# Kernel tuning notes

Measured on AMD Instinct MI355X. Metric: run time of the kernel, lower is better.

## Reference

```python
import jax, jax.numpy as jnp
import numpy as np

B, L, D, K, O, DM = 32, 512, 32, 6, 192, 512
Q = 0.75
EPS = 1e-6
BN_EPS = 1e-5


def _torch_median(a, axis):
    # torch.median returns the LOWER of the two middle values for even n
    n = a.shape[axis]
    s = jnp.sort(a, axis=axis)
    return jnp.take(s, jnp.array([(n - 1) // 2]), axis=axis)


def setup_inputs() -> dict:
    key = jax.random.key(0)
    ks = jax.random.split(key, 5)
    return {
        "x": jax.random.normal(ks[0], (B, L, D), jnp.float32),
        "x_date": jax.random.normal(ks[1], (B, L, D, K), jnp.float32),
        "y_date": jax.random.normal(ks[2], (B, O, D, K), jnp.float32),
        "mlp_w1": jax.random.normal(ks[3], (L, DM), jnp.float32) * 0.02,
        "mlp_b1": jnp.zeros((DM,), jnp.float32),
        "mlp_w2": jax.random.normal(ks[4], (DM, 2), jnp.float32) * 0.02,
        "mlp_b2": jnp.zeros((2,), jnp.float32),
        "bn_gamma": jnp.ones((D,), jnp.float32),
        "bn_beta": jnp.zeros((D,), jnp.float32),
    }


def reference(x, x_date, y_date, mlp_w1, mlp_b1, mlp_w2, mlp_b2, bn_gamma, bn_beta):
    k = x_date.shape[-1]
    # robust location/scale (median + interquantile range), reduced over time dim 1
    med_true = _torch_median(x, 1)                 # (B,1,D)
    med_map = _torch_median(x_date, 1)             # (B,1,D,K)
    std_true = (jnp.quantile(x, Q, axis=1, keepdims=True)
                - jnp.quantile(x, 1.0 - Q, axis=1, keepdims=True) + EPS)   # (B,1,D)
    std_map = (jnp.quantile(x_date, Q, axis=1, keepdims=True)
               - jnp.quantile(x_date, 1.0 - Q, axis=1, keepdims=True) + EPS)  # (B,1,D,K)
    x_date_map = (x_date - med_map) / std_map * std_true[..., None] + med_true[..., None]
    y_date_map = (y_date - med_map) / std_map * std_true[..., None] + med_true[..., None]

    # cross-attention over time with tiny contraction dim k
    scores = jnp.einsum('bldk,bodk->bdlo', x_date_map, y_date_map)  # (B,D,L,O)
    A = jax.nn.softmax(scores / jnp.sqrt(jnp.float32(k)), axis=-2)  # softmax over L
    V = jnp.einsum('bld,bdlo->bdo', x, A)                           # (B,D,O)

    # BatchNorm1d(d_feature) in training mode: batch stats over (B, O); dropout = identity (eval)
    mu = jnp.mean(V, axis=(0, 2), keepdims=True)
    var = jnp.var(V, axis=(0, 2), keepdims=True)
    y = (V - mu) * jax.lax.rsqrt(var + BN_EPS) * bn_gamma[None, :, None] + bn_beta[None, :, None]
    y = jnp.transpose(y, (0, 2, 1))                                 # (B,O,D)

    # softmax-gated fusion MLP over the time axis
    error = x - x_date_map.mean(-1)                                 # (B,L,D)
    h = jax.nn.gelu(jnp.einsum('bld,lm->bdm', error, mlp_w1) + mlp_b1, approximate=False)
    w = jax.nn.softmax(h @ mlp_w2 + mlp_b2, axis=-1)                # (B,D,2)

    y_map = jnp.stack([y_date_map.mean(-1), y], axis=-1)            # (B,O,D,2)
    pred = jnp.sum(y_map * w[:, None], axis=-1)                     # (B,O,D)
    return pred
```

## Files before the change

### kernel.cpp

```cpp
#include <hip/hip_runtime.h>
#include <math.h>

#define BB 32
#define LL 512
#define DD 32
#define KK 6
#define OO 192
#define DM 512

typedef __fp16 h2 __attribute__((ext_vector_type(2)));
union F2H { float f; h2 h; };
__device__ __forceinline__ float asF(h2 h) { F2H u; u.h = h; return u.f; }
__device__ __forceinline__ h2 asH(float f) { F2H u; u.f = f; return u.h; }

typedef short bf16x8 __attribute__((ext_vector_type(8)));
typedef float f4 __attribute__((ext_vector_type(4)));
union U16x8 { uint4 u; bf16x8 h; };

__device__ __forceinline__ unsigned short f2bf(float x) {
  unsigned int u = __float_as_uint(x);
  u = (u + 0x7FFF + ((u >> 16) & 1)) >> 16;
  return (unsigned short)u;
}

#define MOVDPP(x, ctrl) \
  __int_as_float(__builtin_amdgcn_mov_dpp(__float_as_int(x), ctrl, 0xf, 0xf, true))

#define CSTR2 524
#define XD0   0
#define XV0   6288
#define MEDO  7336
#define STDO  7350
#define SAO   7364
#define SCO   7376
#define BNR   7388
#define PK    0
#define DENB  4200
#define NUMB  4968
#define LDSF  7404

__device__ __forceinline__ void sort512(float v[8], int lane) {
  #pragma unroll
  for (int k = 2; k <= 512; k <<= 1) {
    #pragma unroll
    for (int j = k >> 1; j > 0; j >>= 1) {
      if (j >= 8) {
        int jj = j >> 3;
        bool lower = (lane & jj) == 0;
        bool asc = ((lane << 3) & k) == 0;
        bool keepmin = (asc == lower);
        #pragma unroll
        for (int r = 0; r < 8; ++r) {
          float o;
          if (jj == 1)      o = MOVDPP(v[r], 0xB1);
          else if (jj == 2) o = MOVDPP(v[r], 0x4E);
          else if (jj == 8) o = MOVDPP(v[r], 0x128);
          else              o = __shfl_xor(v[r], jj);
          v[r] = keepmin ? fminf(v[r], o) : fmaxf(v[r], o);
        }
      } else {
        #pragma unroll
        for (int r = 0; r < 8; ++r) {
          if ((r & j) == 0) {
            int r2 = r | j;
            bool asc = (((lane << 3) | r) & k) == 0;
            float a = v[r], b = v[r2];
            float lo = fminf(a, b), hi = fmaxf(a, b);
            v[r]  = asc ? lo : hi;
            v[r2] = asc ? hi : lo;
          }
        }
      }
    }
  }
}

__global__ __launch_bounds__(256) void fused_kernel(
    const float* __restrict__ x, const float* __restrict__ x_date,
    const float* __restrict__ y_date, const float* __restrict__ w1,
    float* __restrict__ V, float* __restrict__ ymean,
    float* __restrict__ bnp, unsigned short* __restrict__ errb,
    unsigned short* __restrict__ w1t) {
  __shared__ float lds[LDSF];
  int orig = blockIdx.x;
  int tid = threadIdx.x, lane = tid & 63, wv = tid >> 6;

  if (orig >= 512) {
    float* tw = lds;
    int id = orig - 512;
    int l0 = (id & 7) * 64, m0 = (id >> 3) * 64;
    #pragma unroll
    for (int it = 0; it < 4; ++it) {
      int f = tid + it * 256;
      int row = f >> 4, c4 = f & 15;
      float4 v = ((const float4*)(w1 + (size_t)(l0 + row) * DM + m0))[c4];
      float* p = &tw[row * 68 + c4 * 4];
      p[0] = v.x; p[1] = v.y; p[2] = v.z; p[3] = v.w;
    }
    __syncthreads();
    unsigned int* w1t32 = (unsigned int*)w1t;
    #pragma unroll
    for (int it = 0; it < 8; ++it) {
      int f = tid + it * 256;
      int mr = f >> 5, c = f & 31;
      float a = tw[(c * 2 + 0) * 68 + mr];
      float b = tw[(c * 2 + 1) * 68 + mr];
      unsigned int u = (unsigned int)f2bf(a) | ((unsigned int)f2bf(b) << 16);
      w1t32[(size_t)(m0 + mr) * (DM / 2) + (l0 >> 1) + c] = u;
    }
    return;
  }

  int xcd = orig & 7, idx = orig >> 3;
  int b = (xcd << 2) | (idx >> 4);
  int d0 = (idx & 15) << 1;

  const float* xs = x_date + (size_t)b * LL * 192 + d0 * 6;
  #pragma unroll
  for (int it = 0; it < 6; ++it) {
    int f = tid + it * 256;
    int row = f / 3, c4 = f % 3;
    float4 v = ((const float4*)(xs + (size_t)row * 192))[c4];
    int col = c4 * 4;
    lds[XD0 + (col + 0) * CSTR2 + row] = v.x;
    lds[XD0 + (col + 1) * CSTR2 + row] = v.y;
    lds[XD0 + (col + 2) * CSTR2 + row] = v.z;
    lds[XD0 + (col + 3) * CSTR2 + row] = v.w;
  }
  #pragma unroll
  for (int it = 0; it < 2; ++it) {
    int row = tid + it * 256;
    float2 v = *(const float2*)(x + (size_t)(b * LL + row) * DD + d0);
    lds[XV0 + row]         = v.x;
    lds[XV0 + CSTR2 + row] = v.y;
  }

  int dl = wv >> 1, half = wv & 1;
  int dme = d0 + dl;
  float2 yr[3][3];
  #pragma unroll
  for (int j = 0; j < 3; ++j) {
    const float2* yp = (const float2*)(
        y_date + (((size_t)b * OO + (lane + 64 * j)) * DD + dme) * KK);
    yr[j][0] = yp[0]; yr[j][1] = yp[1]; yr[j][2] = yp[2];
  }
  __syncthreads();

  for (int p = 0; p < 4; ++p) {
    int s = p * 4 + wv;
    if (s < 14) {
      const float4* colp = (s < 12)
          ? (const float4*)&lds[XD0 + s * CSTR2 + lane * 8]
          : (const float4*)&lds[XV0 + (s - 12) * CSTR2 + lane * 8];
      float v[8];
      float4 c0 = colp[0], c1 = colp[1];
      v[0]=c0.x; v[1]=c0.y; v[2]=c0.z; v[3]=c0.w;
      v[4]=c1.x; v[5]=c1.y; v[6]=c1.z; v[7]=c1.w;
      sort512(v, lane);
      float e127 = __shfl(v[7], 15);
      float e128 = __shfl(v[0], 16);
      float e255 = __shfl(v[7], 31);
      float e383 = __shfl(v[7], 47);
      float e384 = __shfl(v[0], 48);
      if (lane == 0) {
        float q25 = e127 + 0.75f * (e128 - e127);
        float q75 = e383 + 0.25f * (e384 - e383);
        lds[MEDO + s] = e255;
        lds[STDO + s] = q75 - q25 + 1e-6f;
      }
    }
  }
  __syncthreads();

  if (tid < 12) {
    int dloc = tid / 6;
    float a = lds[STDO + 12 + dloc] / lds[STDO + tid];
    lds[SAO + tid] = a;
    lds[SCO + tid] = lds[MEDO + 12 + dloc] - lds[MEDO + tid] * a;
  }
  __syncthreads();

  const float PSC = 0.58912435f;

  float4 packed[2][2];
  #pragma unroll
  for (int dli = 0; dli < 2; ++dli) {
    int cb = dli * 6;
    float a0 = lds[SAO+cb+0], a1 = lds[SAO+cb+1], a2 = lds[SAO+cb+2];
    float a3 = lds[SAO+cb+3], a4 = lds[SAO+cb+4], a5 = lds[SAO+cb+5];
    float c0 = lds[SCO+cb+0], c1 = lds[SCO+cb+1], c2 = lds[SCO+cb+2];
    float c3 = lds[SCO+cb+3], c4 = lds[SCO+cb+4], c5 = lds[SCO+cb+5];
    #pragma unroll
    for (int it = 0; it < 2; ++it) {
      int l = tid + it * 256;
      float m0 = a0 * lds[XD0 + (cb + 0) * CSTR2 + l] + c0;
      float m1 = a1 * lds[XD0 + (cb + 1) * CSTR2 + l] + c1;
      float m2 = a2 * lds[XD0 + (cb + 2) * CSTR2 + l] + c2;
      float m3 = a3 * lds[XD0 + (cb + 3) * CSTR2 + l] + c3;
      float m4 = a4 * lds[XD0 + (cb + 4) * CSTR2 + l] + c4;
      float m5 = a5 * lds[XD0 + (cb + 5) * CSTR2 + l] + c5;
      float xvv = lds[XV0 + dli * CSTR2 + l];
      errb[(size_t)((b << 5) | (d0 + dli)) * LL + l] =
          f2bf(xvv - (m0 + m1 + m2 + m3 + m4 + m5) * (1.0f / 6.0f));
      packed[it][dli].x = asF(__builtin_amdgcn_cvt_pkrtz(m0 * PSC, m1 * PSC));
      packed[it][dli].y = asF(__builtin_amdgcn_cvt_pkrtz(m2 * PSC, m3 * PSC));
      packed[it][dli].z = asF(__builtin_amdgcn_cvt_pkrtz(m4 * PSC, m5 * PSC));
      packed[it][dli].w = asF(__builtin_amdgcn_cvt_pkrtz(xvv, 0.0f));
    }
  }
  __syncthreads();

  #pragma unroll
  for (int it = 0; it < 2; ++it) {
    int l = tid + it * 256;
    *(float4*)&lds[PK + 0 * 2048 + l * 4] = packed[it][0];
    *(float4*)&lds[PK + 1 * 2048 + l * 4] = packed[it][1];
  }
  __syncthreads();

  {
    float askw[6], cskw[6];
    #pragma unroll
    for (int k = 0; k < 6; ++k) {
      askw[k] = lds[SAO + dl * 6 + k];
      cskw[k] = lds[SCO + dl * 6 + k];
    }
    h2 yk[3][3];
    #pragma unroll
    for (int j = 0; j < 3; ++j) {
      float q0 = askw[0] * yr[j][0].x + cskw[0];
      float q1 = askw[1] * yr[j][0].y + cskw[1];
      float q2 = askw[2] * yr[j][1].x + cskw[2];
      float q3 = askw[3] * yr[j][1].y + cskw[3];
      float q4 = askw[4] * yr[j][2].x + cskw[4];
      float q5 = askw[5] * yr[j][2].y + cskw[5];
      if (half == 0)
        ymean[(size_t)((b << 5) | dme) * OO + (lane + 64 * j)] =
            (q0 + q1 + q2 + q3 + q4 + q5) * (1.0f / 6.0f);
      yk[j][0] = __builtin_amdgcn_cvt_pkrtz(q0, q1);
      yk[j][1] = __builtin_amdgcn_cvt_pkrtz(q2, q3);
      yk[j][2] = __builtin_amdgcn_cvt_pkrtz(q4, q5);
    }

    float den[3] = {0.f, 0.f, 0.f}, num[3] = {0.f, 0.f, 0.f};
    const float* pk = &lds[PK + dl * 2048 + half * 1024];
    #pragma unroll 4
    for (int l = 0; l < 256; ++l) {
      float4 rw = *(const float4*)&pk[l * 4];
      h2 x01 = asH(rw.x), x23 = asH(rw.y), x45 = asH(rw.z);
      float xf = (float)(asH(rw.w).x);
      #pragma unroll
      for (int j = 0; j < 3; ++j) {
        float sc = __builtin_amdgcn_fdot2(x01, yk[j][0], 0.0f, false);
        sc = __builtin_amdgcn_fdot2(x23, yk[j][1], sc, false);
        sc = __builtin_amdgcn_fdot2(x45, yk[j][2], sc, false);
        float e = exp2f(sc);
        den[j] += e;
        num[j] += e * xf;
      }
    }
    #pragma unroll
    for (int j = 0; j < 3; ++j) {
      lds[DENB + wv * 192 + lane + 64 * j] = den[j];
      lds[NUMB + wv * 192 + lane + 64 * j] = num[j];
    }
  }
  __syncthreads();

  float s1v[2] = {0.f, 0.f}, s2v[2] = {0.f, 0.f};
  if (tid < OO) {
    #pragma unroll
    for (int dli = 0; dli < 2; ++dli) {
      float den = lds[DENB + dli * 384 + tid] + lds[DENB + dli * 384 + 192 + tid];
      float num = lds[NUMB + dli * 384 + tid] + lds[NUMB + dli * 384 + 192 + tid];
      float vv = num / den;
      V[(size_t)((b << 5) | (d0 + dli)) * OO + tid] = vv;
      s1v[dli] = vv; s2v[dli] = vv * vv;
    }
  }
  #pragma unroll
  for (int off = 32; off > 0; off >>= 1) {
    s1v[0] += __shfl_down(s1v[0], off);
    s1v[1] += __shfl_down(s1v[1], off);
    s2v[0] += __shfl_down(s2v[0], off);
    s2v[1] += __shfl_down(s2v[1], off);
  }
  if (lane == 0) {
    lds[BNR + 0  + wv] = s1v[0];
    lds[BNR + 4  + wv] = s1v[1];
    lds[BNR + 8  + wv] = s2v[0];
    lds[BNR + 12 + wv] = s2v[1];
  }
  __syncthreads();
  if (tid == 0) {
    #pragma unroll
    for (int dli = 0; dli < 2; ++dli) {
      float S  = lds[BNR + dli * 4 + 0] + lds[BNR + dli * 4 + 1]
               + lds[BNR + dli * 4 + 2] + lds[BNR + dli * 4 + 3];
      float S2 = lds[BNR + 8 + dli * 4 + 0] + lds[BNR + 8 + dli * 4 + 1]
               + lds[BNR + 8 + dli * 4 + 2] + lds[BNR + 8 + dli * 4 + 3];
      bnp[((d0 + dli) << 5) | b]          = S;
      bnp[1024 + (((d0 + dli) << 5) | b)] = S2;
    }
  }
}

__global__ __launch_bounds__(256) void gate_kernel(
    const unsigned short* __restrict__ errb, const unsigned short* __restrict__ w1t,
    const float* __restrict__ b1, const float* __restrict__ w2,
    float* __restrict__ gatep) {
  __shared__ float part[4][32];
  int orig = blockIdx.x;
  int xcd = orig & 7, idx = orig >> 3;
  int b = (xcd << 2) | (idx >> 3);
  int s = idx & 7;
  int tid = threadIdx.x, lane = tid & 63, wv = tid >> 6;
  int m16 = lane & 15, quad = lane >> 4;
  int mw = s * 64 + wv * 16;
  int r0 = b * 32;

  float b1v = b1[mw + m16];
  float2 w2p = ((const float2*)w2)[mw + m16];
  float w2d = w2p.x - w2p.y;

  f4 acc[2];
  acc[0] = (f4){0.f, 0.f, 0.f, 0.f};
  acc[1] = (f4){0.f, 0.f, 0.f, 0.f};

  const unsigned short* ea = errb + (size_t)(r0 + m16) * DM + quad * 8;
  const unsigned short* eb = ea + 16 * DM;
  const unsigned short* wb = w1t + (size_t)(mw + m16) * DM + quad * 8;

  #pragma unroll
  for (int ks = 0; ks < DM; ks += 32) {
    U16x8 ua0, ua1, ub;
    ua0.u = *(const uint4*)(ea + ks);
    ua1.u = *(const uint4*)(eb + ks);
    ub.u  = *(const uint4*)(wb + ks);
    acc[0] = __builtin_amdgcn_mfma_f32_16x16x32_bf16(ua0.h, ub.h, acc[0], 0, 0, 0);
    acc[1] = __builtin_amdgcn_mfma_f32_16x16x32_bf16(ua1.h, ub.h, acc[1], 0, 0, 0);
  }

  float rsum[2][4];
  #pragma unroll
  for (int rt = 0; rt < 2; ++rt) {
    #pragma unroll
    for (int r = 0; r < 4; ++r) {
      float h = acc[rt][r] + b1v;
      float gg = 0.5f * h * (1.0f + erff(h * 0.70710678f));
      rsum[rt][r] = gg * w2d;
    }
  }
  #pragma unroll
  for (int rt = 0; rt < 2; ++rt) {
    #pragma unroll
    for (int r = 0; r < 4; ++r) {
      rsum[rt][r] += __shfl_xor(rsum[rt][r], 1);
      rsum[rt][r] += __shfl_xor(rsum[rt][r], 2);
      rsum[rt][r] += __shfl_xor(rsum[rt][r], 4);
      rsum[rt][r] += __shfl_xor(rsum[rt][r], 8);
    }
  }
  if (m16 == 0) {
    #pragma unroll
    for (int rt = 0; rt < 2; ++rt)
      #pragma unroll
      for (int r = 0; r < 4; ++r)
        part[wv][rt * 16 + quad * 4 + r] = rsum[rt][r];
  }
  __syncthreads();

  if (tid < 32) {
    float p = part[0][tid] + part[1][tid] + part[2][tid] + part[3][tid];
    gatep[(size_t)(((b << 3) | s) << 5) | tid] = p;
  }
}

__global__ __launch_bounds__(256) void tail_kernel(
    const float* __restrict__ gatep, const float* __restrict__ b2,
    const float* __restrict__ V, const float* __restrict__ ymean,
    const float* __restrict__ bnp,
    const float* __restrict__ gamma, const float* __restrict__ beta,
    float* __restrict__ out) {
  __shared__ float vsh[32 * 28], ysh[32 * 28];
  __shared__ float gsh[32], ssh[32], osh[32];
  int g = blockIdx.x, tid = threadIdx.x;
  int xcd = g & 7, idx = g >> 3;
  int b = (xcd << 2) | (idx >> 3);
  int o0 = (idx & 7) * 24;

  if (tid < 192) {
    int dd = tid / 6, c4 = tid % 6;
    size_t goff = (size_t)(b * DD + dd) * OO + o0;
    float4 v = ((const float4*)(V + goff))[c4];
    float4 y = ((const float4*)(ymean + goff))[c4];
    *(float4*)&vsh[dd * 28 + c4 * 4] = v;
    *(float4*)&ysh[dd * 28 + c4 * 4] = y;
  }

  if (tid < 32) {
    float ld = b2[0] - b2[1];
    #pragma unroll
    for (int s = 0; s < 8; ++s)
      ld += gatep[(size_t)(((b << 3) | s) << 5) | tid];
    gsh[tid] = 1.0f / (1.0f + expf(-ld));
    float S = 0.f, S2 = 0.f;
    const float* pd = bnp + (tid << 5);
    #pragma unroll 8
    for (int bb = 0; bb < 32; ++bb) { S += pd[bb]; S2 += pd[1024 + bb]; }
    const float inv = 1.0f / (BB * OO);
    float mu = S * inv;
    float var = S2 * inv - mu * mu;
    float gg = gamma[tid] * rsqrtf(var + 1e-5f);
    ssh[tid] = gg;
    osh[tid] = beta[tid] - mu * gg;
  }
  __syncthreads();

  if (tid < 192) {
    int op = tid >> 3, c4 = tid & 7;
    float4 r;
    #pragma unroll
    for (int j = 0; j < 4; ++j) {
      int dd = c4 * 4 + j;
      float v  = vsh[dd * 28 + op];
      float ym = ysh[dd * 28 + op];
      float gg = gsh[dd];
      float y  = v * ssh[dd] + osh[dd];
      ((float*)&r)[j] = ym * gg + y * (1.0f - gg);
    }
    ((float4*)(out + (size_t)(b * OO + o0 + op) * DD))[c4] = r;
  }
}

extern "C" void kernel_launch(void* const* d_in, const int* in_sizes, int n_in,
                              void* d_out, int out_size, void* d_ws, size_t ws_size,
                              hipStream_t stream) {
  const float* x      = (const float*)d_in[0];
  const float* x_date = (const float*)d_in[1];
  const float* y_date = (const float*)d_in[2];
  const float* w1     = (const float*)d_in[3];
  const float* b1     = (const float*)d_in[4];
  const float* w2     = (const float*)d_in[5];
  const float* b2     = (const float*)d_in[6];
  const float* gamma  = (const float*)d_in[7];
  const float* beta   = (const float*)d_in[8];
  float* out = (float*)d_out;

  float* ws    = (float*)d_ws;
  float* V     = ws;
  float* ymean = ws + 196608;
  float* bnp   = ws + 393216;
  unsigned short* errb = (unsigned short*)(ws + 395264);
  unsigned short* w1t  = (unsigned short*)(ws + 657408);
  float* gatep = ws + 788480;

  fused_kernel<<<576, 256, 0, stream>>>(x, x_date, y_date, w1,
                                        V, ymean, bnp, errb, w1t);
  gate_kernel<<<256, 256, 0, stream>>>(errb, w1t, b1, w2, gatep);
  tail_kernel<<<256, 256, 0, stream>>>(gatep, b2, V, ymean, bnp,
                                       gamma, beta, out);
}
```

Measured before the change: 145.7 us.

## Compute attention scores with MFMA 16x16x32 f16 instead of fdot2 loops

Replaces the per-lane fdot2 score computation over L with MFMA tiles: mapped x_date and y_date are packed as fp16 into LDS, each wave multiplies 16-row L tiles against six 16-column O tiles, then exponentiates and accumulates den and num. Only lanes with kg==0 feed real data and the rest are zero-padded, so most of the K=32 MFMA depth is wasted. Reductions move to cross-lane shuffles, which drops one LDS round-trip and barrier. The exp2 and accumulation work per score stays the same, so the main saving is in issuing the dot products.

```diff
diff --git a/kernel.cpp b/kernel.cpp
--- a/kernel.cpp
+++ b/kernel.cpp
@@ -9,6 +9,7 @@
 #define DM 512
 
 typedef __fp16 h2 __attribute__((ext_vector_type(2)));
+typedef __fp16 h8 __attribute__((ext_vector_type(8)));
 union F2H { float f; h2 h; };
 __device__ __forceinline__ float asF(h2 h) { F2H u; u.h = h; return u.f; }
 __device__ __forceinline__ h2 asH(float f) { F2H u; u.f = f; return u.h; }
@@ -16,6 +17,7 @@
 typedef short bf16x8 __attribute__((ext_vector_type(8)));
 typedef float f4 __attribute__((ext_vector_type(4)));
 union U16x8 { uint4 u; bf16x8 h; };
+union UH8F { uint4 u; h8 h; };
 
 __device__ __forceinline__ unsigned short f2bf(float x) {
   unsigned int u = __float_as_uint(x);
@@ -34,9 +36,8 @@
 #define SAO   7364
 #define SCO   7376
 #define BNR   7388
-#define PK    0
-#define DENB  4200
-#define NUMB  4968
+#define XMP   0
+#define YMP   4096
 #define LDSF  7404
 
 __device__ __forceinline__ void sort512(float v[8], int lane) {
@@ -138,11 +139,13 @@
   int dl = wv >> 1, half = wv & 1;
   int dme = d0 + dl;
   float2 yr[3][3];
-  #pragma unroll
-  for (int j = 0; j < 3; ++j) {
-    const float2* yp = (const float2*)(
-        y_date + (((size_t)b * OO + (lane + 64 * j)) * DD + dme) * KK);
-    yr[j][0] = yp[0]; yr[j][1] = yp[1]; yr[j][2] = yp[2];
+  if (half == 0) {
+    #pragma unroll
+    for (int j = 0; j < 3; ++j) {
+      const float2* yp = (const float2*)(
+          y_date + (((size_t)b * OO + (lane + 64 * j)) * DD + dme) * KK);
+      yr[j][0] = yp[0]; yr[j][1] = yp[1]; yr[j][2] = yp[2];
+    }
   }
   __syncthreads();
 
@@ -205,7 +208,7 @@
       packed[it][dli].x = asF(__builtin_amdgcn_cvt_pkrtz(m0 * PSC, m1 * PSC));
       packed[it][dli].y = asF(__builtin_amdgcn_cvt_pkrtz(m2 * PSC, m3 * PSC));
       packed[it][dli].z = asF(__builtin_amdgcn_cvt_pkrtz(m4 * PSC, m5 * PSC));
-      packed[it][dli].w = asF(__builtin_amdgcn_cvt_pkrtz(xvv, 0.0f));
+      packed[it][dli].w = 0.0f;
     }
   }
   __syncthreads();
@@ -213,95 +216,106 @@
   #pragma unroll
   for (int it = 0; it < 2; ++it) {
     int l = tid + it * 256;
-    *(float4*)&lds[PK + 0 * 2048 + l * 4] = packed[it][0];
-    *(float4*)&lds[PK + 1 * 2048 + l * 4] = packed[it][1];
-  }
-  __syncthreads();
-
-  {
+    *(float4*)&lds[XMP + (0 * 512 + l) * 4] = packed[it][0];
+    *(float4*)&lds[XMP + (1 * 512 + l) * 4] = packed[it][1];
+  }
+  if (half == 0) {
     float askw[6], cskw[6];
     #pragma unroll
     for (int k = 0; k < 6; ++k) {
       askw[k] = lds[SAO + dl * 6 + k];
       cskw[k] = lds[SCO + dl * 6 + k];
     }
-    h2 yk[3][3];
     #pragma unroll
     for (int j = 0; j < 3; ++j) {
+      int o = lane + 64 * j;
       float q0 = askw[0] * yr[j][0].x + cskw[0];
       float q1 = askw[1] * yr[j][0].y + cskw[1];
       float q2 = askw[2] * yr[j][1].x + cskw[2];
       float q3 = askw[3] * yr[j][1].y + cskw[3];
       float q4 = askw[4] * yr[j][2].x + cskw[4];
       float q5 = askw[5] * yr[j][2].y + cskw[5];
-      if (half == 0)
-        ymean[(size_t)((b << 5) | dme) * OO + (lane + 64 * j)] =
-            (q0 + q1 + q2 + q3 + q4 + q5) * (1.0f / 6.0f);
-      yk[j][0] = __builtin_amdgcn_cvt_pkrtz(q0, q1);
-      yk[j][1] = __builtin_amdgcn_cvt_pkrtz(q2, q3);
-      yk[j][2] = __builtin_amdgcn_cvt_pkrtz(q4, q5);
-    }
-
-    float den[3] = {0.f, 0.f, 0.f}, num[3] = {0.f, 0.f, 0.f};
-    const float* pk = &lds[PK + dl * 2048 + half * 1024];
-    #pragma unroll 4
-    for (int l = 0; l < 256; ++l) {
-      float4 rw = *(const float4*)&pk[l * 4];
-      h2 x01 = asH(rw.x), x23 = asH(rw.y), x45 = asH(rw.z);
-      float xf = (float)(asH(rw.w).x);
+      ymean[(size_t)((b << 5) | dme) * OO + o] =
+          (q0 + q1 + q2 + q3 + q4 + q5) * (1.0f / 6.0f);
+      float4 yq;
+      yq.x = asF(__builtin_amdgcn_cvt_pkrtz(q0, q1));
+      yq.y = asF(__builtin_amdgcn_cvt_pkrtz(q2, q3));
+      yq.z = asF(__builtin_amdgcn_cvt_pkrtz(q4, q5));
+      yq.w = 0.0f;
+      *(float4*)&lds[YMP + (dl * 192 + o) * 4] = yq;
+    }
+  }
+  __syncthreads();
+
+  {
+    int l15 = lane & 15, kg = lane >> 4;
+    uint4 zero4 = make_uint4(0u, 0u, 0u, 0u);
+
+    UH8F bf[6];
+    #pragma unroll
+    for (int ot = 0; ot < 6; ++ot) {
+      int brow = (half * 6 + ot) * 16 + l15;
+      uint4 bu = *(const uint4*)&lds[YMP + (dl * 192 + brow) * 4];
+      bf[ot].u = (kg == 0) ? bu : zero4;
+    }
+
+    float den[6] = {0.f,0.f,0.f,0.f,0.f,0.f};
+    float num[6] = {0.f,0.f,0.f,0.f,0.f,0.f};
+
+    for (int lt = 0; lt < 32; ++lt) {
+      UH8F af;
+      uint4 au = *(const uint4*)&lds[XMP + (dl * 512 + lt * 16 + l15) * 4];
+      af.u = (kg == 0) ? au : zero4;
+      int rbase = lt * 16 + kg * 4;
+      float xv0 = lds[XV0 + dl * CSTR2 + rbase + 0];
+      float xv1 = lds[XV0 + dl * CSTR2 + rbase + 1];
+      float xv2 = lds[XV0 + dl * CSTR2 + rbase + 2];
+      float xv3 = lds[XV0 + dl * CSTR2 + rbase + 3];
       #pragma unroll
-      for (int j = 0; j < 3; ++j) {
-        float sc = __builtin_amdgcn_fdot2(x01, yk[j][0], 0.0f, false);
-        sc = __builtin_amdgcn_fdot2(x23, yk[j][1], sc, false);
-        sc = __builtin_amdgcn_fdot2(x45, yk[j][2], sc, false);
-        float e = exp2f(sc);
-        den[j] += e;
-        num[j] += e * xf;
+      for (int ot = 0; ot < 6; ++ot) {
+        f4 c = __builtin_amdgcn_mfma_f32_16x16x32_f16(
+            af.h, bf[ot].h, (f4){0.f, 0.f, 0.f, 0.f}, 0, 0, 0);
+        float e0 = exp2f(c[0]), e1 = exp2f(c[1]);
+        float e2 = exp2f(c[2]), e3 = exp2f(c[3]);
+        den[ot] += (e0 + e1) + (e2 + e3);
+        num[ot] += (e0 * xv0 + e1 * xv1) + (e2 * xv2 + e3 * xv3);
       }
     }
-    #pragma unroll
-    for (int j = 0; j < 3; ++j) {
-      lds[DENB + wv * 192 + lane + 64 * j] = den[j];
-      lds[NUMB + wv * 192 + lane + 64 * j] = num[j];
-    }
-  }
-  __syncthreads();
-
-  float s1v[2] = {0.f, 0.f}, s2v[2] = {0.f, 0.f};
-  if (tid < OO) {
-    #pragma unroll
-    for (int dli = 0; dli < 2; ++dli) {
-      float den = lds[DENB + dli * 384 + tid] + lds[DENB + dli * 384 + 192 + tid];
-      float num = lds[NUMB + dli * 384 + tid] + lds[NUMB + dli * 384 + 192 + tid];
-      float vv = num / den;
-      V[(size_t)((b << 5) | (d0 + dli)) * OO + tid] = vv;
-      s1v[dli] = vv; s2v[dli] = vv * vv;
-    }
-  }
-  #pragma unroll
-  for (int off = 32; off > 0; off >>= 1) {
-    s1v[0] += __shfl_down(s1v[0], off);
-    s1v[1] += __shfl_down(s1v[1], off);
-    s2v[0] += __shfl_down(s2v[0], off);
-    s2v[1] += __shfl_down(s2v[1], off);
-  }
-  if (lane == 0) {
-    lds[BNR + 0  + wv] = s1v[0];
-    lds[BNR + 4  + wv] = s1v[1];
-    lds[BNR + 8  + wv] = s2v[0];
-    lds[BNR + 12 + wv] = s2v[1];
-  }
-  __syncthreads();
+
+    #pragma unroll
+    for (int ot = 0; ot < 6; ++ot) {
+      den[ot] += __shfl_xor(den[ot], 16);
+      den[ot] += __shfl_xor(den[ot], 32);
+      num[ot] += __shfl_xor(num[ot], 16);
+      num[ot] += __shfl_xor(num[ot], 32);
+    }
+
+    float s1 = 0.f, s2 = 0.f;
+    if (lane < 16) {
+      #pragma unroll
+      for (int ot = 0; ot < 6; ++ot) {
+        float vv = num[ot] / den[ot];
+        V[(size_t)((b << 5) | dme) * OO + half * 96 + ot * 16 + lane] = vv;
+        s1 += vv; s2 += vv * vv;
+      }
+    }
+    s1 += __shfl_xor(s1, 1); s1 += __shfl_xor(s1, 2);
+    s1 += __shfl_xor(s1, 4); s1 += __shfl_xor(s1, 8);
+    s2 += __shfl_xor(s2, 1); s2 += __shfl_xor(s2, 2);
+    s2 += __shfl_xor(s2, 4); s2 += __shfl_xor(s2, 8);
+    if (lane == 0) { lds[BNR + wv] = s1; lds[BNR + 8 + wv] = s2; }
+  }
+  __syncthreads();
+
   if (tid == 0) {
-    #pragma unroll
-    for (int dli = 0; dli < 2; ++dli) {
-      float S  = lds[BNR + dli * 4 + 0] + lds[BNR + dli * 4 + 1]
-               + lds[BNR + dli * 4 + 2] + lds[BNR + dli * 4 + 3];
-      float S2 = lds[BNR + 8 + dli * 4 + 0] + lds[BNR + 8 + dli * 4 + 1]
-               + lds[BNR + 8 + dli * 4 + 2] + lds[BNR + 8 + dli * 4 + 3];
-      bnp[((d0 + dli) << 5) | b]          = S;
-      bnp[1024 + (((d0 + dli) << 5) | b)] = S2;
-    }
+    float S0  = lds[BNR + 0] + lds[BNR + 1];
+    float S20 = lds[BNR + 8 + 0] + lds[BNR + 8 + 1];
+    float S1  = lds[BNR + 2] + lds[BNR + 3];
+    float S21 = lds[BNR + 8 + 2] + lds[BNR + 8 + 3];
+    bnp[(d0 << 5) | b]                = S0;
+    bnp[1024 + ((d0 << 5) | b)]       = S20;
+    bnp[((d0 + 1) << 5) | b]          = S1;
+    bnp[1024 + (((d0 + 1) << 5) | b)] = S21;
   }
 }
 
```

After: 142.5 us. 2.2% less time.
